# Kernel optimization log

Measured on AMD Instinct MI355X. Metric: run time of the kernel, lower is better.

## Reference

```python
import jax, jax.numpy as jnp
import numpy as np

IMG = 800
FEAT_SIZES = [(200, 200), (100, 100), (50, 50), (25, 25)]
STRIDES = [4, 8, 16, 32]
ANCHOR_SIZES = [32, 64, 128, 256]
ASPECTS = np.array([0.5, 1.0, 2.0])
NA = 3
C = 128
PRE_NMS = 2000
POST_NMS = 2000
RPN_NMS_TH = 0.7
BOX_SCORE_TH = 0.05
BOX_NMS_TH = 0.5
DETS = 100
BBOX_CLIP = float(np.log(1000.0 / 16.0))
LVL_H = np.array([h for h, w in FEAT_SIZES], np.int32)
LVL_W = np.array([w for h, w in FEAT_SIZES], np.int32)
LVL_OFF = np.concatenate([[0], np.cumsum(LVL_H * LVL_W)])[:4].astype(np.int32)


def make_anchors():
    out = []
    for (h, w), stride, size in zip(FEAT_SIZES, STRIDES, ANCHOR_SIZES):
        hr = np.sqrt(ASPECTS)
        wr = 1.0 / hr
        ws = wr * size
        hs = hr * size
        base = np.round(np.stack([-ws, -hs, ws, hs], axis=1) / 2.0)  # [NA,4]
        sy = np.arange(h) * stride
        sx = np.arange(w) * stride
        yy, xx = np.meshgrid(sy, sx, indexing='ij')
        shifts = np.stack([xx.ravel(), yy.ravel(), xx.ravel(), yy.ravel()], axis=1)
        out.append((shifts[:, None, :] + base[None, :, :]).reshape(-1, 4))
    return jnp.asarray(np.concatenate(out, 0), jnp.float32)


def decode(deltas, boxes, weights):
    wx, wy, ww, wh = weights
    w = boxes[..., 2] - boxes[..., 0]
    h = boxes[..., 3] - boxes[..., 1]
    cx = boxes[..., 0] + 0.5 * w
    cy = boxes[..., 1] + 0.5 * h
    dx = deltas[..., 0] / wx
    dy = deltas[..., 1] / wy
    dw = jnp.minimum(deltas[..., 2] / ww, BBOX_CLIP)
    dh = jnp.minimum(deltas[..., 3] / wh, BBOX_CLIP)
    pcx = dx * w + cx
    pcy = dy * h + cy
    pw = jnp.exp(dw) * w
    ph = jnp.exp(dh) * h
    return jnp.stack([pcx - 0.5 * pw, pcy - 0.5 * ph, pcx + 0.5 * pw, pcy + 0.5 * ph], axis=-1)


def clip_boxes(b):
    return jnp.stack([jnp.clip(b[..., 0], 0.0, IMG), jnp.clip(b[..., 1], 0.0, IMG),
                      jnp.clip(b[..., 2], 0.0, IMG), jnp.clip(b[..., 3], 0.0, IMG)], axis=-1)


def iou_one_to_many(box, boxes):
    ix1 = jnp.maximum(box[0], boxes[:, 0])
    iy1 = jnp.maximum(box[1], boxes[:, 1])
    ix2 = jnp.minimum(box[2], boxes[:, 2])
    iy2 = jnp.minimum(box[3], boxes[:, 3])
    inter = jnp.maximum(ix2 - ix1, 0.0) * jnp.maximum(iy2 - iy1, 0.0)
    a1 = (box[2] - box[0]) * (box[3] - box[1])
    a2 = (boxes[:, 2] - boxes[:, 0]) * (boxes[:, 3] - boxes[:, 1])
    union = a1 + a2 - inter
    return jnp.where(union > 0, inter / union, 0.0)


def greedy_nms(boxes, scores, th, k):
    def step(sc, _):
        i = jnp.argmax(sc)
        s = sc[i]
        iou = iou_one_to_many(boxes[i], boxes)
        sc = jnp.where(iou > th, -jnp.inf, sc)
        sc = sc.at[i].set(-jnp.inf)
        return sc, (i, s)
    _, (idx, ss) = jax.lax.scan(step, scores, None, length=k)
    return idx, jnp.isfinite(ss)


def conv(x, w, b, pad):
    y = jax.lax.conv_general_dilated(x, w, (1, 1), [(pad, pad), (pad, pad)],
                                     dimension_numbers=('NCHW', 'OIHW', 'NCHW'))
    return y + b[None, :, None, None]


def level_map(rois):
    area = (rois[:, 2] - rois[:, 0]) * (rois[:, 3] - rois[:, 1])
    tgt = jnp.floor(4.0 + jnp.log2(jnp.sqrt(jnp.maximum(area, 0.0)) / 224.0 + 1e-6))
    return (jnp.clip(tgt, 2.0, 5.0) - 2.0).astype(jnp.int32)


def ms_roi_align(flat, rois):
    # flat: [C, total_pixels] concatenation of pyramid levels; rois: [K,4]
    K = rois.shape[0]
    lvl = level_map(rois)
    scale = jnp.asarray(1.0 / np.array(STRIDES), jnp.float32)[lvl]
    Hl = jnp.asarray(LVL_H)[lvl]
    Wl = jnp.asarray(LVL_W)[lvl]
    base = jnp.asarray(LVL_OFF)[lvl]
    x1 = rois[:, 0] * scale
    y1 = rois[:, 1] * scale
    rw = jnp.maximum(rois[:, 2] * scale - x1, 1.0)
    rh = jnp.maximum(rois[:, 3] * scale - y1, 1.0)
    off = jnp.arange(7)[:, None] + (jnp.arange(2) + 0.5)[None, :] / 2.0  # [7,2]
    ys = y1[:, None, None] + off[None] * (rh / 7.0)[:, None, None]  # [K,7,2]
    xs = x1[:, None, None] + off[None] * (rw / 7.0)[:, None, None]
    Y = jnp.broadcast_to(ys[:, :, :, None, None], (K, 7, 2, 7, 2))
    X = jnp.broadcast_to(xs[:, None, None, :, :], (K, 7, 2, 7, 2))
    Hf = Hl.astype(jnp.float32)[:, None, None, None, None]
    Wf = Wl.astype(jnp.float32)[:, None, None, None, None]
    valid = (Y > -1.0) & (Y < Hf) & (X > -1.0) & (X < Wf)
    y = jnp.clip(Y, 0.0, Hf - 1.0)
    x = jnp.clip(X, 0.0, Wf - 1.0)
    y0 = jnp.floor(y).astype(jnp.int32)
    x0 = jnp.floor(x).astype(jnp.int32)
    y1i = jnp.minimum(y0 + 1, (Hl - 1)[:, None, None, None, None])
    x1i = jnp.minimum(x0 + 1, (Wl - 1)[:, None, None, None, None])
    ly = y - y0
    lx = x - x0
    hy = 1.0 - ly
    hx = 1.0 - lx
    Wi = Wl[:, None, None, None, None]
    bi = base[:, None, None, None, None]
    def g(yi, xi):
        return flat[:, (bi + yi * Wi + xi).ravel()]  # [C, K*196]
    v = ((hy * hx).ravel() * g(y0, x0) + (hy * lx).ravel() * g(y0, x1i)
         + (ly * hx).ravel() * g(y1i, x0) + (ly * lx).ravel() * g(y1i, x1i))
    v = jnp.where(valid.ravel()[None, :], v, 0.0)
    v = v.reshape(C, K, 7, 2, 7, 2).mean(axis=(3, 5))  # avg over 2x2 samples
    return v.transpose(1, 0, 2, 3)  # [K,C,7,7]


def forward(feat0, feat1, feat2, feat3, rpn_conv_w, rpn_conv_b, rpn_cls_w, rpn_cls_b,
            rpn_bbox_w, rpn_bbox_b, fc6_w, fc6_b, fc7_w, fc7_b, cls_w, cls_b, bbox_w, bbox_b):
    feats = [feat0, feat1, feat2, feat3]
    anchors = make_anchors()
    level_sizes = [h * w * NA for (h, w) in FEAT_SIZES]
    starts = np.concatenate([[0], np.cumsum(level_sizes)])
    obj_l, del_l = [], []
    for fm in feats:
        t = jax.nn.relu(conv(fm, rpn_conv_w, rpn_conv_b, 1))
        o = conv(t, rpn_cls_w, rpn_cls_b, 0)          # [B,NA,H,W]
        d = conv(t, rpn_bbox_w, rpn_bbox_b, 0)        # [B,4*NA,H,W]
        B, _, H, W = o.shape
        obj_l.append(o.transpose(0, 2, 3, 1).reshape(B, -1))
        del_l.append(d.reshape(B, NA, 4, H, W).transpose(0, 3, 4, 1, 2).reshape(B, -1, 4))
    # torchvision RPN detaches objectness / deltas before proposal generation
    objectness = jax.lax.stop_gradient(jnp.concatenate(obj_l, 1))
    deltas = jax.lax.stop_gradient(jnp.concatenate(del_l, 1))
    proposals = decode(deltas, anchors[None, :, :], (1.0, 1.0, 1.0, 1.0))

    def rpn_filter(obj, props):
        bs, ss, ls = [], [], []
        for li in range(4):
            s, e = int(starts[li]), int(starts[li + 1])
            k = min(PRE_NMS, level_sizes[li])
            vals, idx = jax.lax.top_k(obj[s:e], k)
            bs.append(props[s:e][idx])
            ss.append(vals)
            ls.append(jnp.full((k,), li, jnp.float32))
        boxes = clip_boxes(jnp.concatenate(bs, 0))
        scores = jax.nn.sigmoid(jnp.concatenate(ss, 0))
        lvl = jnp.concatenate(ls, 0)
        ok = (boxes[:, 2] - boxes[:, 0] >= 1e-3) & (boxes[:, 3] - boxes[:, 1] >= 1e-3)
        sm = jnp.where(ok, scores, -jnp.inf)
        idx, keep = greedy_nms(boxes + (lvl * (IMG + 1.0))[:, None], sm, RPN_NMS_TH, POST_NMS)
        return boxes[idx], keep

    prop_boxes, prop_valid = jax.vmap(rpn_filter)(objectness, proposals)

    def head(rois, valid, f0, f1, f2, f3):
        flat = jnp.concatenate([f.reshape(C, -1) for f in (f0, f1, f2, f3)], axis=1)
        pooled = ms_roi_align(flat, rois)               # [K,C,7,7]
        x = pooled.reshape(POST_NMS, -1)
        x = jax.nn.relu(x @ fc6_w.T + fc6_b)
        x = jax.nn.relu(x @ fc7_w.T + fc7_b)
        logits = x @ cls_w.T + cls_b                    # [K,2]
        bdel = (x @ bbox_w.T + bbox_b).reshape(-1, 2, 4)
        boxes_all = clip_boxes(decode(bdel, rois[:, None, :], (10.0, 10.0, 5.0, 5.0)))
        scores_all = jax.nn.softmax(logits, axis=-1)
        bfg = boxes_all[:, 1]
        sfg = scores_all[:, 1]
        keep = valid & (sfg > BOX_SCORE_TH) & (bfg[:, 2] - bfg[:, 0] >= 1e-2) & (bfg[:, 3] - bfg[:, 1] >= 1e-2)
        sm = jnp.where(keep, sfg, -jnp.inf)
        idx, ok = greedy_nms(bfg, sm, BOX_NMS_TH, DETS)
        ob = jnp.where(ok[:, None], bfg[idx], 0.0)
        osc = jnp.where(ok, sfg[idx], 0.0)
        ol = jnp.where(ok, 1, 0).astype(jnp.int32)
        return ob, osc, ol

    return jax.vmap(head)(prop_boxes, prop_valid, feat0, feat1, feat2, feat3)


def setup_inputs():
    key = jax.random.key(0)
    ks = jax.random.split(key, 12)
    def rn(k, shape, s=1.0):
        return jax.random.normal(k, shape, jnp.float32) * s
    return {
        'feat0': rn(ks[0], (2, C, 200, 200)),
        'feat1': rn(ks[1], (2, C, 100, 100)),
        'feat2': rn(ks[2], (2, C, 50, 50)),
        'feat3': rn(ks[3], (2, C, 25, 25)),
        'rpn_conv_w': rn(ks[4], (C, C, 3, 3), 0.02),
        'rpn_conv_b': jnp.zeros((C,), jnp.float32),
        'rpn_cls_w': rn(ks[5], (NA, C, 1, 1), 0.02),
        'rpn_cls_b': jnp.zeros((NA,), jnp.float32),
        'rpn_bbox_w': rn(ks[6], (4 * NA, C, 1, 1), 0.02),
        'rpn_bbox_b': jnp.zeros((4 * NA,), jnp.float32),
        'fc6_w': rn(ks[7], (1024, C * 49), 0.01),
        'fc6_b': jnp.zeros((1024,), jnp.float32),
        'fc7_w': rn(ks[8], (1024, 1024), 0.01),
        'fc7_b': jnp.zeros((1024,), jnp.float32),
        'cls_w': rn(ks[9], (2, 1024), 0.01),
        'cls_b': jnp.zeros((2,), jnp.float32),
        'bbox_w': rn(ks[10], (8, 1024), 0.001),
        'bbox_b': jnp.zeros((8,), jnp.float32),
    }


def reference(feat0, feat1, feat2, feat3, rpn_conv_w, rpn_conv_b, rpn_cls_w, rpn_cls_b,
              rpn_bbox_w, rpn_bbox_b, fc6_w, fc6_b, fc7_w, fc7_b, cls_w, cls_b, bbox_w, bbox_b):
    return forward(feat0, feat1, feat2, feat3, rpn_conv_w, rpn_conv_b, rpn_cls_w, rpn_cls_b,
                   rpn_bbox_w, rpn_bbox_b, fc6_w, fc6_b, fc7_w, fc7_b, cls_w, cls_b, bbox_w, bbox_b)
```

## Files before the change

kernel.cpp:

```cpp
#include <hip/hip_runtime.h>
#include <cmath>

static constexpr int kAImg = 159375;
static constexpr int kNCand = 7875;
static constexpr int kPostNms = 2000;
static constexpr int kMPad = 2048;
static constexpr int kHWCImg = 53125;
static constexpr float kISC = 1.0f / 4096.0f;

__constant__ int c_AOFF[4]   = {0, 120000, 150000, 157500};
__constant__ int c_ALVL[4]   = {120000, 30000, 7500, 1875};
__constant__ int c_CBASE[4]  = {0, 2000, 4000, 6000};
__constant__ int c_LW[4]     = {200, 100, 50, 25};
__constant__ int c_LH[4]     = {200, 100, 50, 25};
__constant__ int c_STRIDE[4] = {4, 8, 16, 32};
__constant__ int c_POFF[4]   = {0, 40000, 50000, 52500};
__constant__ int c_JCHUNK[9] = {0, 118, 148, 156, 158, 276, 306, 314, 316};

struct Cand     { float x1, y1, x2, y2; unsigned key; unsigned lvl; unsigned pad0, pad1; };
struct HeadCand { float x1, y1, x2, y2; float score; unsigned key; unsigned pad0, pad1; };
struct RoiParam { int lvl; float x1, y1, rw, rh; int pad0, pad1, pad2; };
struct AnchTab  { float v[4][3][4]; };

typedef unsigned short u16;
typedef __attribute__((ext_vector_type(8))) short short8;
typedef __attribute__((ext_vector_type(4))) float f32x4;
typedef _Float16 f16x8 __attribute__((ext_vector_type(8)));

__device__ __forceinline__ unsigned keyOf(float f) {
  unsigned u = __float_as_uint(f);
  return (u & 0x80000000u) ? ~u : (u | 0x80000000u);
}

__device__ __forceinline__ void split_f16(float f, u16& hi, u16& lo) {
  union { _Float16 h; u16 u; } a, b;
  a.h = (_Float16)f;
  float r = (f - (float)a.h) * 4096.0f;
  b.h = (_Float16)r;
  hi = a.u; lo = b.u;
}

__device__ __forceinline__ unsigned long long shfl64(unsigned long long v, int src) {
  int lo = __shfl((int)(unsigned)(v & 0xffffffffull), src);
  int hi = __shfl((int)(unsigned)(v >> 32), src);
  return ((unsigned long long)(unsigned)hi << 32) | (unsigned)lo;
}

__device__ __forceinline__ float iou_pair(float4 a, float4 b) {
#pragma clang fp contract(off)
  float ix1 = fmaxf(a.x, b.x), iy1 = fmaxf(a.y, b.y);
  float ix2 = fminf(a.z, b.z), iy2 = fminf(a.w, b.w);
  float iw = fmaxf(ix2 - ix1, 0.f), ih = fmaxf(iy2 - iy1, 0.f);
  float inter = iw * ih;
  float a1 = (a.z - a.x) * (a.w - a.y);
  float a2 = (b.z - b.x) * (b.w - b.y);
  float uni = a1 + a2 - inter;
  return uni > 0.f ? inter / uni : 0.f;
}

__device__ __forceinline__ float4 decode_clip(float bx1, float by1, float bx2, float by2,
                                              float d0, float d1, float d2, float d3,
                                              float wx, float wy, float ww, float wh) {
#pragma clang fp contract(off)
  float w = bx2 - bx1, h = by2 - by1;
  float cx = bx1 + 0.5f * w, cy = by1 + 0.5f * h;
  float dx = d0 / wx, dy = d1 / wy;
  float dw = fminf(d2 / ww, 4.135166556742356f);
  float dh = fminf(d3 / wh, 4.135166556742356f);
  float pcx = dx * w + cx, pcy = dy * h + cy;
  float pw = expf(dw) * w, ph = expf(dh) * h;
  float x1 = pcx - 0.5f * pw, y1 = pcy - 0.5f * ph;
  float x2 = pcx + 0.5f * pw, y2 = pcy + 0.5f * ph;
  x1 = fminf(fmaxf(x1, 0.f), 800.f); y1 = fminf(fmaxf(y1, 0.f), 800.f);
  x2 = fminf(fmaxf(x2, 0.f), 800.f); y2 = fminf(fmaxf(y2, 0.f), 800.f);
  return make_float4(x1, y1, x2, y2);
}

__device__ __forceinline__ unsigned block_scan_bool(bool p, unsigned* wbuf, unsigned& total) {
  unsigned long long m = __ballot(p);
  int lane = threadIdx.x & 63;
  int wid = threadIdx.x >> 6;
  unsigned exc = (unsigned)__popcll(m & ((lane == 0) ? 0ull : ((~0ull) >> (64 - lane))));
  if (lane == 0) wbuf[wid] = (unsigned)__popcll(m);
  __syncthreads();
  unsigned pre = 0, tot = 0;
#pragma unroll
  for (int w = 0; w < 16; w++) { unsigned c = wbuf[w]; if (w < wid) pre += c; tot += c; }
  total = tot;
  __syncthreads();
  return pre + exc;
}

__global__ __launch_bounds__(256) void zero_u32_kernel(unsigned* __restrict__ p, int n32) {
  for (int i = blockIdx.x * 256 + threadIdx.x; i < n32; i += gridDim.x * 256) p[i] = 0u;
}

template <int H, int W>
__global__ __launch_bounds__(256) void transpose_pad_kernel(
    const float* __restrict__ feat, u16* __restrict__ Fh, u16* __restrict__ Fl,
    float* __restrict__ Fw) {
  __shared__ float tile[128][65];
  int y = blockIdx.y;
  int x0 = blockIdx.x * 64;
  for (int e = threadIdx.x; e < 128 * 64; e += 256) {
    int ci = e >> 6, x = e & 63;
    float v = 0.f;
    if (x0 + x < W) v = feat[(size_t)ci * (H * W) + y * W + x0 + x];
    tile[ci][x] = v;
  }
  __syncthreads();
  for (int e = threadIdx.x; e < 64 * 128; e += 256) {
    int x = e >> 7, ci = e & 127;
    if (x0 + x >= W) continue;
    float v = tile[ci][x];
    u16 hi, lo;
    split_f16(v, hi, lo);
    size_t out = ((size_t)(y + 1) * (W + 2) + (x0 + x + 1)) * 128 + ci;
    Fh[out] = hi; Fl[out] = lo;
    Fw[((size_t)y * W + (x0 + x)) * 128 + ci] = v;
  }
}

__global__ __launch_bounds__(256) void conv_w_repack_kernel(
    const float* __restrict__ w3, u16* __restrict__ Wh, u16* __restrict__ Wl) {
  int idx = blockIdx.x * 256 + threadIdx.x;
  if (idx >= 9 * 128 * 128) return;
  int tap = idx >> 14;
  int r = idx & 16383;
  int co = r >> 7, ci = r & 127;
  u16 hi, lo;
  split_f16(w3[co * 1152 + ci * 9 + tap], hi, lo);
  Wh[idx] = hi; Wl[idx] = lo;
}

template <int H, int W>
__global__ __launch_bounds__(256) void conv_mfma_kernel(
    const u16* __restrict__ Fh, const u16* __restrict__ Fl,
    const u16* __restrict__ Wh, const u16* __restrict__ Wl,
    const float* __restrict__ b3, float* __restrict__ tbuf) {
  __shared__ u16 sAh[128][40], sAl[128][40], sBh[128][40], sBl[128][40];
  int tid = threadIdx.x;
  int m0 = blockIdx.x * 128;
  int w = tid >> 6, lane = tid & 63;
  int wm = (w >> 1) * 64, wn = (w & 1) * 64;
  int quad = lane >> 4, lrow = lane & 15;
  f32x4 acc1[4][4], acc2[4][4];
#pragma unroll
  for (int i = 0; i < 4; i++)
#pragma unroll
    for (int j = 0; j < 4; j++) { acc1[i][j] = (f32x4)0.f; acc2[i][j] = (f32x4)0.f; }

  for (int tap = 0; tap < 9; tap++) {
    int ky = tap / 3, kx = tap - (tap / 3) * 3;
    for (int c = 0; c < 4; c++) {
      for (int e = tid; e < 512; e += 256) {
        int row = e >> 2, seg = (e & 3) * 8;
        int m = m0 + row;
        int y = m / W, x = m - y * W;
// ... 131 lines not shown
  int n = c_ALVL[l];
  int i = chunk * 1024 + (int)threadIdx.x;
  bool act = i < n;
  unsigned key = act ? keys[(size_t)b * kAImg + c_AOFF[l] + i] : 0u;
  unsigned T = (l == 3) ? 0u : tkT[b * 4 + l];
  bool gt = act && (l != 3) && (key > T);
  bool eq = act && (l != 3) && (key == T);
  unsigned long long mg = __ballot(gt), me = __ballot(eq);
  int lane = threadIdx.x & 63, wid = threadIdx.x >> 6;
  if (lane == 0) { wg[wid] = (unsigned)__popcll(mg); we[wid] = (unsigned)__popcll(me); }
  __syncthreads();
  if (threadIdx.x == 0) {
    unsigned g = 0, e = 0;
#pragma unroll
    for (int t = 0; t < 16; t++) { g += wg[t]; e += we[t]; }
    gtCnt[cb] = g; eqCnt[cb] = e;
  }
}

__global__ __launch_bounds__(512) void cand_prefix_kernel(
    unsigned* __restrict__ gtCnt, unsigned* __restrict__ eqCnt,
    unsigned* __restrict__ gtBase, unsigned* __restrict__ eqBase) {
  int j = threadIdx.x >> 6;
  int lane = threadIdx.x & 63;
  if (lane != 0) return;
  int c0 = c_JCHUNK[j], c1 = c_JCHUNK[j + 1];
  unsigned g = 0, e = 0;
  for (int c = c0; c < c1; c++) {
    gtBase[c] = g; eqBase[c] = e;
    g += gtCnt[c]; e += eqCnt[c];
  }
}

__global__ __launch_bounds__(1024) void cand_scatter_kernel(
    const unsigned* __restrict__ keys, const float* __restrict__ deltas,
    const unsigned* __restrict__ tkT, const unsigned* __restrict__ tkNeed,
    const unsigned* __restrict__ gtBase, const unsigned* __restrict__ eqBase,
    Cand* __restrict__ cand, AnchTab tab) {
  __shared__ unsigned wbuf[16];
  int cb = blockIdx.x;
  int j = 0;
#pragma unroll
  for (int t = 1; t < 8; t++) if (cb >= c_JCHUNK[t]) j = t;
  int chunk = cb - c_JCHUNK[j];
  int b = j >> 2, l = j & 3;
  int n = c_ALVL[l];
  int W = c_LW[l];
  int stride = c_STRIDE[l];
  const float* db = deltas + ((size_t)b * kAImg + c_AOFF[l]) * 4;
  Cand* cbuf = cand + (size_t)b * kNCand + c_CBASE[l];
  bool selAll = (l == 3);
  unsigned T = selAll ? 0u : tkT[b * 4 + l];
  unsigned need = selAll ? 0u : tkNeed[b * 4 + l];
  int i = chunk * 1024 + (int)threadIdx.x;
  bool act = i < n;
  unsigned key = act ? keys[(size_t)b * kAImg + c_AOFF[l] + i] : 0u;
  bool gt = act && !selAll && (key > T);
  bool eq = act && !selAll && (key == T);
  unsigned tmp;
  unsigned gtExc = block_scan_bool(gt, wbuf, tmp);
  unsigned eqExc = block_scan_bool(eq, wbuf, tmp);
  unsigned gtCount = gtBase[cb] + gtExc;
  unsigned eqCount = eqBase[cb] + eqExc;
  bool isSel = act && (selAll || gt || (eq && eqCount < need));
  if (!isSel) return;
  int slot = selAll ? i : (int)(gtCount + (eqCount < need ? eqCount : need));
  int pos = i / 3, a = i - pos * 3;
  int yy = pos / W, xx = pos - yy * W;
  float sx = (float)(xx * stride), sy = (float)(yy * stride);
  float ax1 = tab.v[l][a][0] + sx;
  float ay1 = tab.v[l][a][1] + sy;
  float ax2 = tab.v[l][a][2] + sx;
  float ay2 = tab.v[l][a][3] + sy;
  float d0 = db[(size_t)i * 4 + 0], d1 = db[(size_t)i * 4 + 1];
  float d2 = db[(size_t)i * 4 + 2], d3 = db[(size_t)i * 4 + 3];
  float4 bx = decode_clip(ax1, ay1, ax2, ay2, d0, d1, d2, d3, 1.f, 1.f, 1.f, 1.f);
  bool ok = (bx.z - bx.x >= 0.001f) && (bx.w - bx.y >= 0.001f);
  Cand cd;
  cd.x1 = bx.x; cd.y1 = bx.y; cd.x2 = bx.z; cd.y2 = bx.w;
  cd.key = ok ? key : 0u; cd.lvl = (unsigned)l; cd.pad0 = 0; cd.pad1 = 0;
  cbuf[slot] = cd;
}

template <int NPAD>
__global__ __launch_bounds__(1024) void sort_desc_kernel(
    const unsigned* __restrict__ keyBase, int strideWords, int nFixed,
    const unsigned* __restrict__ nPtr, unsigned* __restrict__ sortedSlot,
    unsigned* __restrict__ validCnt, int imgStrideKeyWords, int imgStrideSlot) {
  __shared__ unsigned sk[NPAD];
  __shared__ unsigned short sslot[NPAD];
  __shared__ unsigned s_cnt;
  int b = blockIdx.x;
  const unsigned* kbase = keyBase + (size_t)b * imgStrideKeyWords;
  unsigned* oslot = sortedSlot + (size_t)b * imgStrideSlot;
  unsigned* ocnt = validCnt + b;
  int n = nFixed;
  if (nPtr) { int m = (int)nPtr[b]; n = n < m ? n : m; }
  for (int i = threadIdx.x; i < NPAD; i += 1024) {
    sk[i] = (i < n) ? kbase[(size_t)i * strideWords] : 0u;
    sslot[i] = (unsigned short)i;
  }
  if (threadIdx.x == 0) s_cnt = 0;
  __syncthreads();
  for (int k2 = 2; k2 <= NPAD; k2 <<= 1) {
    for (int j = k2 >> 1; j > 0; j >>= 1) {
      for (int i = threadIdx.x; i < NPAD; i += 1024) {
        int ixj = i ^ j;
        if (ixj > i) {
          unsigned ka = sk[i], kb2 = sk[ixj];
          unsigned short sa = sslot[i], sb = sslot[ixj];
          bool aGreater = (ka > kb2) || (ka == kb2 && sa < sb);
          bool up = ((i & k2) == 0);
          bool doSwap = up ? (!aGreater) : aGreater;
          if (doSwap) { sk[i] = kb2; sk[ixj] = ka; sslot[i] = sb; sslot[ixj] = sa; }
        }
      }
      __syncthreads();
    }
  }
  unsigned local = 0;
  for (int i = threadIdx.x; i < NPAD; i += 1024) {
    oslot[i] = (unsigned)sslot[i];
    if (sk[i] > 0u) local++;
  }
  atomicAdd(&s_cnt, local);
  __syncthreads();
  if (threadIdx.x == 0) *ocnt = s_cnt;
}

__global__ __launch_bounds__(256) void rpn_sort_gather(
    const Cand* __restrict__ cand, const unsigned* __restrict__ ss,
    const unsigned* __restrict__ validCnt, float4* __restrict__ boxRaw) {
  int b = blockIdx.y;
  int pos = blockIdx.x * 256 + threadIdx.x;
  int valid = (int)validCnt[b];
  float4 raw = make_float4(0.f, 0.f, 0.f, 0.f);
  if (pos < valid) {
    Cand c = cand[(size_t)b * kNCand + ss[(size_t)b * 8192 + pos]];
    raw = make_float4(c.x1, c.y1, c.x2, c.y2);
  }
  boxRaw[(size_t)b * 8192 + pos] = raw;
}

__global__ __launch_bounds__(1024) void lvl_compact_kernel(
    const Cand* __restrict__ cand, const unsigned* __restrict__ ss,
    const unsigned* __restrict__ validCnt, float4* __restrict__ boxLvl,
    unsigned* __restrict__ lvlList, unsigned* __restrict__ lvlCnt) {
  int b = blockIdx.x;
  int valid = (int)validCnt[b];
  __shared__ unsigned wbuf[16];
  __shared__ unsigned s_run;
  for (int l = 0; l < 4; l++) {
    if (threadIdx.x == 0) s_run = 0;
    __syncthreads();
    for (int c0 = 0; c0 < 8192; c0 += 1024) {
      int pos = c0 + (int)threadIdx.x;
      bool act = pos < valid;
      unsigned lv = 99u;
      float4 off4 = make_float4(0.f, 0.f, 0.f, 0.f);
      if (act) {
#pragma clang fp contract(off)
        Cand c = cand[(size_t)b * kNCand + ss[(size_t)b * 8192 + pos]];
        lv = c.lvl;
        float off = 801.0f * (float)c.lvl;
        off4 = make_float4(c.x1 + off, c.y1 + off, c.x2 + off, c.y2 + off);
      }
      bool isl = act && (lv == (unsigned)l);
      unsigned tot;
      unsigned exc = block_scan_bool(isl, wbuf, tot);
      unsigned run = s_run;
      if (isl) {
        unsigned slot = run + exc;
        lvlList[((size_t)b * 4 + l) * 2048 + slot] = (unsigned)pos;
        boxLvl[((size_t)b * 4 + l) * 2048 + slot] = off4;
      }
      __syncthreads();
      if (threadIdx.x == 0) s_run = run + tot;
      __syncthreads();
    }
    if (threadIdx.x == 0) lvlCnt[b * 4 + l] = s_run;
    __syncthreads();
  }
}

__global__ __launch_bounds__(256) void head_sort_gather(
    const HeadCand* __restrict__ hc, const unsigned* __restrict__ hsorted,
    const unsigned* __restrict__ hvalid, float4* __restrict__ hbox, float* __restrict__ hsc) {
  int pos = blockIdx.x * 256 + threadIdx.x;
  int valid = (int)*hvalid;
  float4 v = make_float4(0.f, 0.f, 0.f, 0.f);
  float s = 0.f;
  if (pos < valid) {
    HeadCand c = hc[hsorted[pos]];
    v = make_float4(c.x1, c.y1, c.x2, c.y2);
    s = c.score;
  }
  hbox[pos] = v;
  hsc[pos] = s;
}

__global__ __launch_bounds__(64) void nms_mask_kernel(
    const float4* __restrict__ boxesOff, const unsigned* __restrict__ validCnt,
    unsigned long long* __restrict__ mask, int rowStrideWords,
    int imgBoxStride, long long imgMaskStride, float th) {
  int b = blockIdx.z;
  const float4* bx = boxesOff + (size_t)b * imgBoxStride;
  unsigned long long* mrow = mask + (size_t)b * imgMaskStride;
  int valid = (int)validCnt[b];
  int i = blockIdx.x * 64 + threadIdx.x;
  int j0 = blockIdx.y * 64;
  __shared__ float4 sb[64];
  sb[threadIdx.x] = bx[j0 + threadIdx.x];
  __syncthreads();
  float4 a = bx[i];
  unsigned long long bits = 0;
  for (int t = 0; t < 64; t++) {
    int j = j0 + t;
    if (j > i && j < valid && iou_pair(a, sb[t]) > th) bits |= (1ull << t);
  }
  mrow[(size_t)i * rowStrideWords + (j0 >> 6)] = bits;
}

__global__ __launch_bounds__(64) void nms_col_kernel(
    const float4* __restrict__ boxes, const unsigned* __restrict__ validCnt,
    unsigned long long* __restrict__ colw, int jobBoxStride, int jobColStride, float th) {
  int job = blockIdx.y;
  int base = blockIdx.x * 64;
  const float4* bx = boxes + (size_t)job * jobBoxStride;
  int valid = (int)validCnt[job];
  int lane = threadIdx.x;
  __shared__ float4 sb[64];
  sb[lane] = bx[base + lane];
  __syncthreads();
  float4 a = sb[lane];
  unsigned long long bits = 0;
  if (base + lane < valid) {
    for (int t = 0; t < lane; t++) {
      if (iou_pair(sb[t], a) > th) bits |= (1ull << t);
    }
  }
  colw[(size_t)job * jobColStride + base + lane] = bits;
}

template <int KMAX>
__global__ __launch_bounds__(64) void nms_reduce_frontier_kernel(
    const unsigned long long* __restrict__ mask,
    const unsigned long long* __restrict__ colw,
    const unsigned* __restrict__ validCnt,
    unsigned* __restrict__ keptIdx, unsigned* __restrict__ keptCnt,
    long long jobMaskStride, int jobColStride) {
  int job = blockIdx.x;
  const unsigned long long* mrow = mask + (size_t)job * jobMaskStride;
  const unsigned long long* mcol = colw + (size_t)job * jobColStride;
  int valid = (int)validCnt[job];
  unsigned* kout = keptIdx + (size_t)job * KMAX;
  int lane = threadIdx.x;
  int half = lane >> 5, w = lane & 31;
  unsigned long long removed = 0ull;
  int keptTotal = 0;
  int ntiles = (valid + 63) >> 6;

  unsigned long long pf[32];
  unsigned long long colNext = 0ull;
  auto issue = [&](int k) {
    int base = k * 64;
#pragma unroll
    for (int i = 0; i < 32; i++) {
      int r = base + 2 * i + half;
      pf[i] = (r < valid) ? mrow[(size_t)r * 32 + w] : 0ull;
    }
    colNext = (base + lane < valid) ? mcol[base + lane] : 0ull;
  };
  if (ntiles > 0) issue(0);

  for (int k = 0; k < ntiles; k++) {
    int base = k * 64;
    int nt = valid - base; if (nt > 64) nt = 64;
    unsigned long long col = colNext;
    unsigned long long Wrm = shfl64(removed, k);
    bool dead = (lane >= nt) || (((Wrm >> lane) & 1ull) != 0ull);
    bool kept = false;
    unsigned long long Kb = 0ull, Db = __ballot(dead);
    while (~(Kb | Db) != 0ull) {
      if (!kept && !dead) {
        if (col & Kb) dead = true;
        else if ((col & ~Db) == 0ull) kept = true;
      }
      Kb = __ballot(kept);
      Db = __ballot(dead);
    }
    int tk = __popcll(Kb);
    bool full = false;
    if (keptTotal + tk > KMAX) {
      int drop = keptTotal + tk - KMAX;
      unsigned long long kk = Kb;
      for (int d = 0; d < drop; d++) kk &= ~(1ull << (63 - __builtin_clzll(kk)));
      Kb = kk; tk = KMAX - keptTotal; full = true;
    }
    if (lane == 0) {
      unsigned long long km = Kb;
      int kc = keptTotal;
      while (km) { int t = __builtin_ctzll(km); km &= km - 1; kout[kc++] = (unsigned)(base + t); }
    }
    keptTotal += tk;
    if (full) break;
    unsigned long long acc = 0ull;
    unsigned long long kb = Kb >> half;
#pragma unroll
    for (int i = 0; i < 32; i++) {
      if ((kb >> (2 * i)) & 1ull) acc |= pf[i];
    }
    unsigned long long accOther = shfl64(acc, (lane + 32) & 63);
    if (lane < 32) removed |= acc | accOther;
    if (k + 1 < ntiles) issue(k + 1);
  }
  if (lane == 0) keptCnt[job] = (unsigned)keptTotal;
}

__global__ __launch_bounds__(256) void flag_scatter_kernel(
    const unsigned* __restrict__ keptLoc, const unsigned* __restrict__ lvlKeptCnt,
    const unsigned* __restrict__ lvlList, unsigned char* __restrict__ kflag) {
  int job = blockIdx.y;
  int k = blockIdx.x * 256 + threadIdx.x;
  if (k >= (int)lvlKeptCnt[job]) return;
  unsigned local = keptLoc[(size_t)job * 2048 + k];
  unsigned pos = lvlList[(size_t)job * 2048 + local];
  int b = job >> 2;
  kflag[(size_t)b * 8192 + pos] = 1;
}

__global__ __launch_bounds__(1024) void merge_kept_kernel(
    const unsigned char* __restrict__ kflag, const unsigned* __restrict__ validCnt,
    unsigned* __restrict__ keptIdx, unsigned* __restrict__ Mc) {
  int b = blockIdx.x;
  int valid = (int)validCnt[b];
  __shared__ unsigned wbuf[16];
  __shared__ unsigned s_run;
  if (threadIdx.x == 0) s_run = 0;
  __syncthreads();
  for (int c0 = 0; c0 < 8192; c0 += 1024) {
    int i = c0 + (int)threadIdx.x;
    bool k = (i < valid) && kflag[(size_t)b * 8192 + i];
    unsigned tot;
    unsigned exc = block_scan_bool(k, wbuf, tot);
    unsigned run = s_run;
    if (k) {
      unsigned slot = run + exc;
      if (slot < kPostNms) keptIdx[(size_t)b * kPostNms + slot] = (unsigned)i;
    }
    __syncthreads();
    if (threadIdx.x == 0) s_run = run + tot;
    __syncthreads();
  }
  if (threadIdx.x == 0) {
    unsigned r = s_run;
    Mc[b] = r < kPostNms ? r : kPostNms;
  }
}

__global__ __launch_bounds__(256) void rpn_roi_gather(
    const unsigned* __restrict__ keptIdx, const unsigned* __restrict__ Mc,
    const float4* __restrict__ boxRaw, float* __restrict__ rois) {
  int b = blockIdx.y;
  int k = blockIdx.x * 256 + threadIdx.x;
  if (k >= (int)Mc[b]) return;
  unsigned i = keptIdx[(size_t)b * kPostNms + k];
  float4 v = boxRaw[(size_t)b * 8192 + i];
  float* r = rois + ((size_t)b * kPostNms + k) * 4;
  r[0] = v.x; r[1] = v.y; r[2] = v.z; r[3] = v.w;
}

__global__ __launch_bounds__(128) void head_det_gather(
    const unsigned* __restrict__ keptIdx, const unsigned* __restrict__ cnt,
    const float4* __restrict__ hbox, const float* __restrict__ hsc,
    float* __restrict__ detBox, float* __restrict__ detSc) {
  int k = threadIdx.x;
  if (k >= (int)*cnt || k >= 100) return;
  unsigned i = keptIdx[k];
  float4 v = hbox[i];
  detBox[k * 4 + 0] = v.x; detBox[k * 4 + 1] = v.y;
  detBox[k * 4 + 2] = v.z; detBox[k * 4 + 3] = v.w;
  detSc[k] = hsc[i];
}

__global__ __launch_bounds__(256) void roi_params_kernel(
    const float* __restrict__ rois, const unsigned* __restrict__ Mc, RoiParam* __restrict__ par) {
  int b = blockIdx.y;
  int i = blockIdx.x * 256 + threadIdx.x;
  if (i >= (int)Mc[b]) return;
  const float* r = rois + ((size_t)b * kPostNms + i) * 4;
  float x1 = r[0], y1 = r[1], x2 = r[2], y2 = r[3];
  float area = (x2 - x1) * (y2 - y1);
  float tgt = floorf(4.0f + log2f(sqrtf(fmaxf(area, 0.f)) / 224.0f + 1e-6f));
  tgt = fminf(fmaxf(tgt, 2.f), 5.f);
  int l = (int)tgt - 2;
  const float scales[4] = {0.25f, 0.125f, 0.0625f, 0.03125f};
  float sc = scales[l];
  RoiParam p;
  p.lvl = l;
  p.x1 = x1 * sc; p.y1 = y1 * sc;
  p.rw = fmaxf(x2 * sc - p.x1, 1.0f);
  p.rh = fmaxf(y2 * sc - p.y1, 1.0f);
  p.pad0 = p.pad1 = p.pad2 = 0;
  par[(size_t)b * kPostNms + i] = p;
}

__global__ __launch_bounds__(256) void pad_pooled_kernel(
    u16* __restrict__ hi, u16* __restrict__ lo, const unsigned* __restrict__ Mc, int b) {
  int start = (int)Mc[b] * 6272;
// ... 183 lines not shown
  }
}

__global__ __launch_bounds__(256) void head_decode_kernel(
    const float* __restrict__ out10, const float* __restrict__ rois,
    const unsigned* __restrict__ Mc, HeadCand* __restrict__ hc, int b) {
#pragma clang fp contract(off)
  int r = blockIdx.x * 256 + threadIdx.x;
  if (r >= (int)Mc[b]) return;
  const float* h = out10 + (size_t)r * 10;
  float l0 = h[0], l1 = h[1];
  float mx = fmaxf(l0, l1);
  float e0 = expf(l0 - mx), e1 = expf(l1 - mx);
  float sfg = e1 / (e0 + e1);
  const float* rr = rois + ((size_t)b * kPostNms + r) * 4;
  float4 bx = decode_clip(rr[0], rr[1], rr[2], rr[3], h[6], h[7], h[8], h[9],
                          10.f, 10.f, 5.f, 5.f);
  bool keep = (sfg > 0.05f) && (bx.z - bx.x >= 0.01f) && (bx.w - bx.y >= 0.01f);
  HeadCand c;
  c.x1 = bx.x; c.y1 = bx.y; c.x2 = bx.z; c.y2 = bx.w;
  c.score = sfg;
  c.key = keep ? keyOf(sfg) : 0u;
  c.pad0 = c.pad1 = 0;
  hc[r] = c;
}

__global__ __launch_bounds__(256) void output_kernel(
    const float* __restrict__ detBox, const float* __restrict__ detSc,
    const unsigned* __restrict__ detCnt, float* __restrict__ out) {
  int t = threadIdx.x;
  if (t >= 200) return;
  int b = t / 100, q = t - b * 100;
  int cnt = (int)detCnt[b];
  float bx0 = 0.f, bx1 = 0.f, bx2 = 0.f, bx3 = 0.f, sc = 0.f, lb = 0.f;
  if (q < cnt) {
    const float* d = detBox + ((size_t)b * 100 + q) * 4;
    bx0 = d[0]; bx1 = d[1]; bx2 = d[2]; bx3 = d[3];
    sc = detSc[b * 100 + q];
    lb = 1.0f;
  }
  float* ob = out + ((size_t)b * 100 + q) * 4;
  ob[0] = bx0; ob[1] = bx1; ob[2] = bx2; ob[3] = bx3;
  out[800 + t] = sc;
  out[1000 + t] = lb;
}

extern "C" void kernel_launch(void* const* d_in, const int* in_sizes, int n_in,
                              void* d_out, int out_size, void* d_ws, size_t ws_size,
                              hipStream_t stream) {
  (void)in_sizes; (void)n_in; (void)out_size; (void)ws_size;
  const float* feats[4] = {(const float*)d_in[0], (const float*)d_in[1],
                           (const float*)d_in[2], (const float*)d_in[3]};
  const float* w3 = (const float*)d_in[4];
  const float* b3 = (const float*)d_in[5];
  const float* wc = (const float*)d_in[6];
  const float* bcs = (const float*)d_in[7];
  const float* wb = (const float*)d_in[8];
  const float* bbx = (const float*)d_in[9];
  const float* fc6w = (const float*)d_in[10];
  const float* fc6b = (const float*)d_in[11];
  const float* fc7w = (const float*)d_in[12];
  const float* fc7b = (const float*)d_in[13];
  const float* clsw = (const float*)d_in[14];
  const float* clsb = (const float*)d_in[15];
  const float* bboxw = (const float*)d_in[16];
  const float* bboxb = (const float*)d_in[17];

  unsigned char* base = (unsigned char*)d_ws;
  size_t off = 0;
  auto alloc = [&](size_t bytes) -> void* {
    void* p = base + off;
    off += (bytes + 255) & ~(size_t)255;
    return p;
  };
  unsigned* keys = (unsigned*)alloc((size_t)2 * kAImg * 4);
  float* deltas = (float*)alloc((size_t)2 * kAImg * 16);
  unsigned* tkT = (unsigned*)alloc(32);
  unsigned* tkNeed = (unsigned*)alloc(32);
  unsigned* gtCnt = (unsigned*)alloc(316 * 4);
  unsigned* eqCnt = (unsigned*)alloc(316 * 4);
  unsigned* gtBase = (unsigned*)alloc(316 * 4);
  unsigned* eqBase = (unsigned*)alloc(316 * 4);
  Cand* cand = (Cand*)alloc((size_t)2 * kNCand * sizeof(Cand));
  unsigned* sortedSlot = (unsigned*)alloc((size_t)2 * 8192 * 4);
  unsigned* validCnt = (unsigned*)alloc(8);
  float4* boxRaw = (float4*)alloc((size_t)2 * 8192 * 16);
  float4* boxLvl = (float4*)alloc((size_t)8 * 2048 * 16);
  unsigned* lvlList = (unsigned*)alloc((size_t)8 * 2048 * 4);
  unsigned* lvlCnt = (unsigned*)alloc(32);
  unsigned long long* lvlMask = (unsigned long long*)alloc((size_t)8 * 2048 * 32 * 8);
  unsigned long long* lvlCol = (unsigned long long*)alloc((size_t)8 * 2048 * 8);
  unsigned* keptLoc = (unsigned*)alloc((size_t)8 * 2048 * 4);
  unsigned* lvlKeptCnt = (unsigned*)alloc(32);
  unsigned char* kflag = (unsigned char*)alloc((size_t)2 * 8192);
  unsigned* keptIdx = (unsigned*)alloc((size_t)2 * kPostNms * 4);
  float* rois = (float*)alloc((size_t)2 * kPostNms * 16);
  unsigned* Mc = (unsigned*)alloc(8);
  RoiParam* roiPar = (RoiParam*)alloc((size_t)2 * kPostNms * sizeof(RoiParam));
  u16* padHi = (u16*)alloc((size_t)204 * 202 * 128 * 2);
  u16* padLo = (u16*)alloc((size_t)204 * 202 * 128 * 2);
  u16* wTapHi = (u16*)alloc((size_t)9 * 128 * 128 * 2);
  u16* wTapLo = (u16*)alloc((size_t)9 * 128 * 128 * 2);
  float* tbuf = (float*)alloc((size_t)313 * 128 * 128 * 4);
  float* fhwc = (float*)alloc((size_t)2 * kHWCImg * 128 * 4);
  u16* pooledHi = (u16*)alloc((size_t)kMPad * 6272 * 2);
  u16* pooledLo = (u16*)alloc((size_t)kMPad * 6272 * 2);
  u16* fc6wHi = (u16*)alloc((size_t)1024 * 6272 * 2);
  u16* fc6wLo = (u16*)alloc((size_t)1024 * 6272 * 2);
  u16* fc7wHi = (u16*)alloc((size_t)1024 * 1024 * 2);
  u16* fc7wLo = (u16*)alloc((size_t)1024 * 1024 * 2);
  float* part = (float*)alloc((size_t)2 * kMPad * 1024 * 4);
  u16* H1hi = (u16*)alloc((size_t)kMPad * 1024 * 2);
  u16* H1lo = (u16*)alloc((size_t)kMPad * 1024 * 2);
  float* H2buf = (float*)alloc((size_t)kMPad * 1024 * 4);
  float* out10 = (float*)alloc((size_t)kPostNms * 10 * 4);
  HeadCand* hc = (HeadCand*)alloc((size_t)kPostNms * sizeof(HeadCand));
  unsigned* hsorted = (unsigned*)alloc((size_t)2048 * 4);
  unsigned* hvalid = (unsigned*)alloc(4);
  float4* hbox = (float4*)alloc((size_t)2048 * 16);
  float* hsc = (float*)alloc((size_t)2048 * 4);
  unsigned long long* hMask = (unsigned long long*)alloc((size_t)2048 * 32 * 8);
  unsigned long long* hCol = (unsigned long long*)alloc((size_t)2048 * 8);
  unsigned* hkept = (unsigned*)alloc((size_t)128 * 4);
  float* detBox = (float*)alloc((size_t)2 * 100 * 4 * 4);
  float* detSc = (float*)alloc((size_t)2 * 100 * 4);
  unsigned* detCnt = (unsigned*)alloc(8);

  AnchTab tab;
  {
    const double aspects[3] = {0.5, 1.0, 2.0};
    const int sizes[4] = {32, 64, 128, 256};
    for (int l = 0; l < 4; l++)
      for (int a = 0; a < 3; a++) {
        double hr = sqrt(aspects[a]);
        double wr = 1.0 / hr;
        double wsz = wr * sizes[l], hsz = hr * sizes[l];
        tab.v[l][a][0] = (float)rint(-wsz / 2.0);
        tab.v[l][a][1] = (float)rint(-hsz / 2.0);
        tab.v[l][a][2] = (float)rint(wsz / 2.0);
        tab.v[l][a][3] = (float)rint(hsz / 2.0);
      }
  }

  const int LH[4] = {200, 100, 50, 25}, LW[4] = {200, 100, 50, 25};
  const int AOFF[4] = {0, 120000, 150000, 157500};
  const int POFF[4] = {0, 40000, 50000, 52500};

  convert_split_fc6_kernel<<<(1024 * 6272 + 255) / 256, 256, 0, stream>>>(fc6w, fc6wHi, fc6wLo);
  convert_split_kernel<<<1024, 256, 0, stream>>>(fc7w, fc7wHi, fc7wLo, 1024 * 1024);
  conv_w_repack_kernel<<<(9 * 128 * 128 + 255) / 256, 256, 0, stream>>>(w3, wTapHi, wTapLo);

  for (int b = 0; b < 2; b++) {
    for (int l = 0; l < 4; l++) {
      int H = LH[l], W = LW[l];
      int HW = H * W;
      int mtiles = (HW + 127) / 128;
      int n32 = (H + 4) * (W + 2) * 128 / 2;
      zero_u32_kernel<<<512, 256, 0, stream>>>((unsigned*)padHi, n32);
      zero_u32_kernel<<<512, 256, 0, stream>>>((unsigned*)padLo, n32);
      const float* fsrc = feats[l] + (size_t)b * 128 * HW;
      float* fdst = fhwc + ((size_t)b * kHWCImg + POFF[l]) * 128;
      dim3 tgrid((W + 63) / 64, H);
      switch (l) {
        case 0:
          transpose_pad_kernel<200, 200><<<tgrid, 256, 0, stream>>>(fsrc, padHi, padLo, fdst);
          conv_mfma_kernel<200, 200><<<mtiles, 256, 0, stream>>>(padHi, padLo, wTapHi, wTapLo, b3, tbuf);
          break;
        case 1:
          transpose_pad_kernel<100, 100><<<tgrid, 256, 0, stream>>>(fsrc, padHi, padLo, fdst);
          conv_mfma_kernel<100, 100><<<mtiles, 256, 0, stream>>>(padHi, padLo, wTapHi, wTapLo, b3, tbuf);
          break;
        case 2:
          transpose_pad_kernel<50, 50><<<tgrid, 256, 0, stream>>>(fsrc, padHi, padLo, fdst);
          conv_mfma_kernel<50, 50><<<mtiles, 256, 0, stream>>>(padHi, padLo, wTapHi, wTapLo, b3, tbuf);
          break;
        default:
          transpose_pad_kernel<25, 25><<<tgrid, 256, 0, stream>>>(fsrc, padHi, padLo, fdst);
          conv_mfma_kernel<25, 25><<<mtiles, 256, 0, stream>>>(padHi, padLo, wTapHi, wTapLo, b3, tbuf);
          break;
      }
      head_1x1_kernel<<<(HW + 255) / 256, 256, 0, stream>>>(
          tbuf, wc, bcs, wb, bbx, keys + (size_t)b * kAImg,
          deltas + (size_t)b * kAImg * 4, AOFF[l], HW);
    }
  }

  radix_select_kernel<<<6, 1024, 0, stream>>>(keys, tkT, tkNeed);
  cand_count_kernel<<<316, 1024, 0, stream>>>(keys, tkT, gtCnt, eqCnt);
  cand_prefix_kernel<<<1, 512, 0, stream>>>(gtCnt, eqCnt, gtBase, eqBase);
  cand_scatter_kernel<<<316, 1024, 0, stream>>>(
      keys, deltas, tkT, tkNeed, gtBase, eqBase, cand, tab);
  sort_desc_kernel<8192><<<2, 1024, 0, stream>>>(
      ((const unsigned*)cand) + 4, 8, kNCand, nullptr, sortedSlot, validCnt, kNCand * 8, 8192);
  rpn_sort_gather<<<dim3(32, 2), 256, 0, stream>>>(cand, sortedSlot, validCnt, boxRaw);
  lvl_compact_kernel<<<2, 1024, 0, stream>>>(cand, sortedSlot, validCnt, boxLvl, lvlList, lvlCnt);
  nms_mask_kernel<<<dim3(32, 32, 8), 64, 0, stream>>>(
      boxLvl, lvlCnt, lvlMask, 32, 2048, (long long)2048 * 32, 0.7f);
  nms_col_kernel<<<dim3(32, 8), 64, 0, stream>>>(
      boxLvl, lvlCnt, lvlCol, 2048, 2048, 0.7f);
  nms_reduce_frontier_kernel<2048><<<8, 64, 0, stream>>>(
      lvlMask, lvlCol, lvlCnt, keptLoc, lvlKeptCnt, (long long)2048 * 32, 2048);
  zero_u32_kernel<<<16, 256, 0, stream>>>((unsigned*)kflag, 4096);
  flag_scatter_kernel<<<dim3(8, 8), 256, 0, stream>>>(keptLoc, lvlKeptCnt, lvlList, kflag);
  merge_kept_kernel<<<2, 1024, 0, stream>>>(kflag, validCnt, keptIdx, Mc);
  rpn_roi_gather<<<dim3(8, 2), 256, 0, stream>>>(keptIdx, Mc, boxRaw, rois);
  roi_params_kernel<<<dim3(8, 2), 256, 0, stream>>>(rois, Mc, roiPar);

  for (int b = 0; b < 2; b++) {
    pad_pooled_kernel<<<512, 256, 0, stream>>>(pooledHi, pooledLo, Mc, b);
    roi_align_hwc_kernel<<<(kPostNms * 49 + 3) / 4, 256, 0, stream>>>(
        fhwc, roiPar + (size_t)b * kPostNms, Mc, pooledHi, pooledLo, b);
    gemm_f16x3_kernel<<<dim3(8, 16, 2), 256, 0, stream>>>(
        pooledHi, pooledLo, fc6wHi, fc6wLo, part, 6272, 98);
    combine_relu_split_kernel<<<8192, 256, 0, stream>>>(part, fc6b, H1hi, H1lo);
    gemm_f16x3_kernel<<<dim3(8, 16, 2), 256, 0, stream>>>(
        H1hi, H1lo, fc7wHi, fc7wLo, part, 1024, 16);
    combine_relu_f32_kernel<<<8192, 256, 0, stream>>>(part, fc7b, H2buf);
    head_linear_kernel<<<2000, 64, 0, stream>>>(H2buf, clsw, clsb, bboxw, bboxb, Mc + b, out10);
    head_decode_kernel<<<8, 256, 0, stream>>>(out10, rois, Mc, hc, b);
    sort_desc_kernel<2048><<<1, 1024, 0, stream>>>(
        ((const unsigned*)hc) + 5, 8, 2000, Mc + b, hsorted, hvalid, 0, 0);
    head_sort_gather<<<8, 256, 0, stream>>>(hc, hsorted, hvalid, hbox, hsc);
    nms_mask_kernel<<<dim3(32, 32, 1), 64, 0, stream>>>(
        hbox, hvalid, hMask, 32, 0, 0, 0.5f);
    nms_col_kernel<<<dim3(32, 1), 64, 0, stream>>>(
        hbox, hvalid, hCol, 0, 0, 0.5f);
    nms_reduce_frontier_kernel<100><<<1, 64, 0, stream>>>(
        hMask, hCol, hvalid, hkept, detCnt + b, (long long)2048 * 32, 0);
    head_det_gather<<<1, 128, 0, stream>>>(
        hkept, detCnt + b, hbox, hsc, detBox + (size_t)b * 400, detSc + (size_t)b * 100);
  }
  output_kernel<<<1, 256, 0, stream>>>(detBox, detSc, detCnt, (float*)d_out);
}
```

Before: 2.203 ms.

## Sort RPN candidates per level and merge ranks via binary search

Replaces the single 8192-element bitonic sort per image, plus the serial level-compaction kernel, with eight parallel 2048-element per-level sorts. Each element's global rank comes from binary searches over the other levels' sorted key arrays, using tie-breaking that matches the original order. This targets a long serial sort on only two blocks and a 32-iteration scan loop, and replaces them with more blocks and less work. It risks diverging from the original order if ties across levels are not broken the same way.

Result: faster. 2.049 ms (-7.0%).

```diff
diff --git a/kernel.cpp b/kernel.cpp
--- a/kernel.cpp
+++ b/kernel.cpp
@@ -11,6 +11,7 @@
 __constant__ int c_AOFF[4]   = {0, 120000, 150000, 157500};
 __constant__ int c_ALVL[4]   = {120000, 30000, 7500, 1875};
 __constant__ int c_CBASE[4]  = {0, 2000, 4000, 6000};
+__constant__ int c_NLVL[4]   = {2000, 2000, 2000, 1875};
 __constant__ int c_LW[4]     = {200, 100, 50, 25};
 __constant__ int c_LH[4]     = {200, 100, 50, 25};
 __constant__ int c_STRIDE[4] = {4, 8, 16, 32};
@@ -74,6 +75,17 @@
   x1 = fminf(fmaxf(x1, 0.f), 800.f); y1 = fminf(fmaxf(y1, 0.f), 800.f);
   x2 = fminf(fmaxf(x2, 0.f), 800.f); y2 = fminf(fmaxf(y2, 0.f), 800.f);
   return make_float4(x1, y1, x2, y2);
+}
+
+__device__ __forceinline__ int cnt_gt(const unsigned* __restrict__ arr, int n, unsigned k) {
+  int lo = 0, hi = n;
+  while (lo < hi) { int mid = (lo + hi) >> 1; if (arr[mid] > k) lo = mid + 1; else hi = mid; }
+  return lo;
+}
+__device__ __forceinline__ int cnt_ge(const unsigned* __restrict__ arr, int n, unsigned k) {
+  int lo = 0, hi = n;
+  while (lo < hi) { int mid = (lo + hi) >> 1; if (arr[mid] >= k) lo = mid + 1; else hi = mid; }
+  return lo;
 }
 
 __device__ __forceinline__ unsigned block_scan_bool(bool p, unsigned* wbuf, unsigned& total) {
@@ -371,6 +383,85 @@
   cbuf[slot] = cd;
 }
 
+__global__ __launch_bounds__(1024) void lvl_sort_kernel(
+    const Cand* __restrict__ cand, unsigned* __restrict__ lvlKeys,
+    unsigned* __restrict__ lvlSlot, unsigned* __restrict__ lvlCnt) {
+  __shared__ unsigned sk[2048];
+  __shared__ unsigned short ss[2048];
+  __shared__ unsigned s_cnt;
+  int job = blockIdx.x;
+  int b = job >> 2, l = job & 3;
+  const Cand* seg = cand + (size_t)b * kNCand + c_CBASE[l];
+  int n = c_NLVL[l];
+  for (int i = threadIdx.x; i < 2048; i += 1024) {
+    sk[i] = (i < n) ? seg[i].key : 0u;
+    ss[i] = (unsigned short)i;
+  }
+  if (threadIdx.x == 0) s_cnt = 0;
+  __syncthreads();
+  for (int k2 = 2; k2 <= 2048; k2 <<= 1) {
+    for (int j = k2 >> 1; j > 0; j >>= 1) {
+      for (int i = threadIdx.x; i < 2048; i += 1024) {
+        int ixj = i ^ j;
+        if (ixj > i) {
+          unsigned ka = sk[i], kb2 = sk[ixj];
+          unsigned short sa = ss[i], sb = ss[ixj];
+          bool aGreater = (ka > kb2) || (ka == kb2 && sa < sb);
+          bool up = ((i & k2) == 0);
+          bool doSwap = up ? (!aGreater) : aGreater;
+          if (doSwap) { sk[i] = kb2; sk[ixj] = ka; ss[i] = sb; ss[ixj] = sa; }
+        }
+      }
+      __syncthreads();
+    }
+  }
+  unsigned local = 0;
+  for (int i = threadIdx.x; i < 2048; i += 1024) {
+    lvlKeys[(size_t)job * 2048 + i] = sk[i];
+    lvlSlot[(size_t)job * 2048 + i] = (unsigned)ss[i];
+    if (sk[i] > 0u) local++;
+  }
+  atomicAdd(&s_cnt, local);
+  __syncthreads();
+  if (threadIdx.x == 0) lvlCnt[job] = s_cnt;
+}
+
+__global__ __launch_bounds__(256) void rank_box_kernel(
+    const Cand* __restrict__ cand, const unsigned* __restrict__ lvlKeys,
+    const unsigned* __restrict__ lvlSlot, const unsigned* __restrict__ lvlCnt,
+    float4* __restrict__ boxLvl, unsigned* __restrict__ gposOf,
+    float4* __restrict__ boxRaw) {
+  int job = blockIdx.y;
+  int b = job >> 2, l = job & 3;
+  int i = blockIdx.x * 256 + threadIdx.x;
+  if (i >= (int)lvlCnt[job]) return;
+  unsigned k = lvlKeys[(size_t)job * 2048 + i];
+  int gpos = i;
+  for (int l2 = 0; l2 < 4; l2++) {
+    if (l2 == l) continue;
+    const unsigned* arr = lvlKeys + (size_t)(b * 4 + l2) * 2048;
+    int n2 = (int)lvlCnt[b * 4 + l2];
+    gpos += (l2 < l) ? cnt_ge(arr, n2, k) : cnt_gt(arr, n2, k);
+  }
+  unsigned slot = lvlSlot[(size_t)job * 2048 + i];
+  Cand c = cand[(size_t)b * kNCand + c_CBASE[l] + slot];
+  {
+#pragma clang fp contract(off)
+    float off = 801.0f * (float)l;
+    boxLvl[(size_t)job * 2048 + i] = make_float4(c.x1 + off, c.y1 + off, c.x2 + off, c.y2 + off);
+  }
+  gposOf[(size_t)job * 2048 + i] = (unsigned)gpos;
+  boxRaw[(size_t)b * 8192 + gpos] = make_float4(c.x1, c.y1, c.x2, c.y2);
+}
+
+__global__ __launch_bounds__(64) void total_valid_kernel(
+    const unsigned* __restrict__ lvlCnt, unsigned* __restrict__ validCnt) {
+  if (threadIdx.x < 2) {
+    int b = threadIdx.x;
+    validCnt[b] = lvlCnt[b * 4] + lvlCnt[b * 4 + 1] + lvlCnt[b * 4 + 2] + lvlCnt[b * 4 + 3];
+  }
+}
+
 template <int NPAD>
 __global__ __launch_bounds__(1024) void sort_desc_kernel(
     const unsigned* __restrict__ keyBase, int strideWords, int nFixed,
@@ -417,61 +508,6 @@
   if (threadIdx.x == 0) *ocnt = s_cnt;
 }
 
-__global__ __launch_bounds__(256) void rpn_sort_gather(
-    const Cand* __restrict__ cand, const unsigned* __restrict__ ss,
-    const unsigned* __restrict__ validCnt, float4* __restrict__ boxRaw) {
-  int b = blockIdx.y;
-  int pos = blockIdx.x * 256 + threadIdx.x;
-  int valid = (int)validCnt[b];
-  float4 raw = make_float4(0.f, 0.f, 0.f, 0.f);
-  if (pos < valid) {
-    Cand c = cand[(size_t)b * kNCand + ss[(size_t)b * 8192 + pos]];
-    raw = make_float4(c.x1, c.y1, c.x2, c.y2);
-  }
-  boxRaw[(size_t)b * 8192 + pos] = raw;
-}
-
-__global__ __launch_bounds__(1024) void lvl_compact_kernel(
-    const Cand* __restrict__ cand, const unsigned* __restrict__ ss,
-    const unsigned* __restrict__ validCnt, float4* __restrict__ boxLvl,
-    unsigned* __restrict__ lvlList, unsigned* __restrict__ lvlCnt) {
-  int b = blockIdx.x;
-  int valid = (int)validCnt[b];
-  __shared__ unsigned wbuf[16];
-  __shared__ unsigned s_run;
-  for (int l = 0; l < 4; l++) {
-    if (threadIdx.x == 0) s_run = 0;
-    __syncthreads();
-    for (int c0 = 0; c0 < 8192; c0 += 1024) {
-      int pos = c0 + (int)threadIdx.x;
-      bool act = pos < valid;
-      unsigned lv = 99u;
-      float4 off4 = make_float4(0.f, 0.f, 0.f, 0.f);
-      if (act) {
-#pragma clang fp contract(off)
-        Cand c = cand[(size_t)b * kNCand + ss[(size_t)b * 8192 + pos]];
-        lv = c.lvl;
-        float off = 801.0f * (float)c.lvl;
-        off4 = make_float4(c.x1 + off, c.y1 + off, c.x2 + off, c.y2 + off);
-      }
-      bool isl = act && (lv == (unsigned)l);
-      unsigned tot;
-      unsigned exc = block_scan_bool(isl, wbuf, tot);
-      unsigned run = s_run;
-      if (isl) {
-        unsigned slot = run + exc;
-        lvlList[((size_t)b * 4 + l) * 2048 + slot] = (unsigned)pos;
-        boxLvl[((size_t)b * 4 + l) * 2048 + slot] = off4;
-      }
-      __syncthreads();
-      if (threadIdx.x == 0) s_run = run + tot;
-      __syncthreads();
-    }
-    if (threadIdx.x == 0) lvlCnt[b * 4 + l] = s_run;
-    __syncthreads();
-  }
-}
-
 __global__ __launch_bounds__(256) void head_sort_gather(
     const HeadCand* __restrict__ hc, const unsigned* __restrict__ hsorted,
     const unsigned* __restrict__ hvalid, float4* __restrict__ hbox, float* __restrict__ hsc) {
@@ -608,12 +644,12 @@
 
 __global__ __launch_bounds__(256) void flag_scatter_kernel(
     const unsigned* __restrict__ keptLoc, const unsigned* __restrict__ lvlKeptCnt,
-    const unsigned* __restrict__ lvlList, unsigned char* __restrict__ kflag) {
+    const unsigned* __restrict__ gposOf, unsigned char* __restrict__ kflag) {
   int job = blockIdx.y;
   int k = blockIdx.x * 256 + threadIdx.x;
   if (k >= (int)lvlKeptCnt[job]) return;
   unsigned local = keptLoc[(size_t)job * 2048 + k];
-  unsigned pos = lvlList[(size_t)job * 2048 + local];
+  unsigned pos = gposOf[(size_t)job * 2048 + local];
   int b = job >> 2;
   kflag[(size_t)b * 8192 + pos] = 1;
 }
@@ -963,12 +999,13 @@
   unsigned* gtBase = (unsigned*)alloc(316 * 4);
   unsigned* eqBase = (unsigned*)alloc(316 * 4);
   Cand* cand = (Cand*)alloc((size_t)2 * kNCand * sizeof(Cand));
-  unsigned* sortedSlot = (unsigned*)alloc((size_t)2 * 8192 * 4);
+  unsigned* lvlKeys = (unsigned*)alloc((size_t)8 * 2048 * 4);
+  unsigned* lvlSlot = (unsigned*)alloc((size_t)8 * 2048 * 4);
+  unsigned* lvlCnt = (unsigned*)alloc(32);
+  unsigned* gposOf = (unsigned*)alloc((size_t)8 * 2048 * 4);
   unsigned* validCnt = (unsigned*)alloc(8);
   float4* boxRaw = (float4*)alloc((size_t)2 * 8192 * 16);
   float4* boxLvl = (float4*)alloc((size_t)8 * 2048 * 16);
-  unsigned* lvlList = (unsigned*)alloc((size_t)8 * 2048 * 4);
-  unsigned* lvlCnt = (unsigned*)alloc(32);
   unsigned long long* lvlMask = (unsigned long long*)alloc((size_t)8 * 2048 * 32 * 8);
   unsigned long long* lvlCol = (unsigned long long*)alloc((size_t)8 * 2048 * 8);
   unsigned* keptLoc = (unsigned*)alloc((size_t)8 * 2048 * 4);
@@ -1071,10 +1108,10 @@
   cand_prefix_kernel<<<1, 512, 0, stream>>>(gtCnt, eqCnt, gtBase, eqBase);
   cand_scatter_kernel<<<316, 1024, 0, stream>>>(
       keys, deltas, tkT, tkNeed, gtBase, eqBase, cand, tab);
-  sort_desc_kernel<8192><<<2, 1024, 0, stream>>>(
-      ((const unsigned*)cand) + 4, 8, kNCand, nullptr, sortedSlot, validCnt, kNCand * 8, 8192);
-  rpn_sort_gather<<<dim3(32, 2), 256, 0, stream>>>(cand, sortedSlot, validCnt, boxRaw);
-  lvl_compact_kernel<<<2, 1024, 0, stream>>>(cand, sortedSlot, validCnt, boxLvl, lvlList, lvlCnt);
+  lvl_sort_kernel<<<8, 1024, 0, stream>>>(cand, lvlKeys, lvlSlot, lvlCnt);
+  rank_box_kernel<<<dim3(8, 8), 256, 0, stream>>>(
+      cand, lvlKeys, lvlSlot, lvlCnt, boxLvl, gposOf, boxRaw);
+  total_valid_kernel<<<1, 64, 0, stream>>>(lvlCnt, validCnt);
   nms_mask_kernel<<<dim3(32, 32, 8), 64, 0, stream>>>(
       boxLvl, lvlCnt, lvlMask, 32, 2048, (long long)2048 * 32, 0.7f);
   nms_col_kernel<<<dim3(32, 8), 64, 0, stream>>>(
@@ -1082,7 +1119,7 @@
   nms_reduce_frontier_kernel<2048><<<8, 64, 0, stream>>>(
       lvlMask, lvlCol, lvlCnt, keptLoc, lvlKeptCnt, (long long)2048 * 32, 2048);
   zero_u32_kernel<<<16, 256, 0, stream>>>((unsigned*)kflag, 4096);
-  flag_scatter_kernel<<<dim3(8, 8), 256, 0, stream>>>(keptLoc, lvlKeptCnt, lvlList, kflag);
+  flag_scatter_kernel<<<dim3(8, 8), 256, 0, stream>>>(keptLoc, lvlKeptCnt, gposOf, kflag);
   merge_kept_kernel<<<2, 1024, 0, stream>>>(kflag, validCnt, keptIdx, Mc);
   rpn_roi_gather<<<dim3(8, 2), 256, 0, stream>>>(keptIdx, Mc, boxRaw, rois);
   roi_params_kernel<<<dim3(8, 2), 256, 0, stream>>>(rois, Mc, roiPar);
```
